# Kernel tuning notes

Hardware: AMD Instinct MI355X
Metric: run time of the kernel (lower is better)

The kernel has to match this reference:

```python
import jax, jax.numpy as jnp
import numpy as np

B, L, D, K = 32, 128, 400, 40
RTOL, ATOL = 1e-4, 1e-6


def setup_inputs() -> dict:
    key = jax.random.key(0)
    ks = jax.random.split(key, 9)
    s = 0.3                      # input scale keeps exp(energy) in fp32 range
    u = 1.0 / np.sqrt(D)         # param scale
    input_h = jax.random.normal(ks[0], (B, L, D), jnp.float32) * s
    input_c = jax.random.normal(ks[1], (B, L, D), jnp.float32) * s
    W_d = jax.random.normal(ks[2], (K, D), jnp.float32) * u
    W_e = jax.random.normal(ks[3], (K, D), jnp.float32) * u
    U = jax.random.normal(ks[4], (K, D, D), jnp.float32) * u
    b = jax.random.normal(ks[5], (K,), jnp.float32) * 0.1
    heads = jax.random.randint(ks[6], (B, L), 0, L)
    pos = jnp.arange(L)[None, :]
    heads = jnp.where(heads == pos, (heads + 1) % L, heads)  # no self-loops (diag is -inf)
    arc_tags = jax.random.randint(ks[7], (B, L), 0, K)
    lengths = jax.random.randint(ks[8], (B,), L // 2, L + 1)
    mask = (jnp.arange(L)[None, :] < lengths[:, None]).astype(jnp.float32)
    return {"input_h": input_h, "input_c": input_c, "W_d": W_d, "W_e": W_e,
            "U": U, "b": b, "mask": mask, "heads": heads,
            "arc_tags": arc_tags, "lengths": lengths}


def reference(input_h, input_c, W_d, W_e, U, b, mask, heads, arc_tags, lengths):
    Bsz, Ln, _ = input_h.shape
    # --- BiAAttention: energy[b,k,head,child] ---
    bil = jnp.einsum('bhd,kde,bce->bkhc', input_h, U, input_c)
    sd = jnp.einsum('kd,bhd->bkh', W_d, input_h)[:, :, :, None]   # head bias
    se = jnp.einsum('kd,bcd->bkc', W_e, input_c)[:, :, None, :]   # child bias
    energy = bil + sd + se + b[None, :, None, None]
    energy = energy * mask[:, None, :, None] * mask[:, None, None, :]
    eye = jnp.eye(Ln, dtype=energy.dtype)
    energy = energy + jnp.where(eye > 0, -jnp.inf, 0.0)           # no self-arcs
    # --- Matrix-Tree partition function ---
    A = jnp.exp(energy) * mask[:, None, :, None] * mask[:, None, None, :]
    A = A.sum(axis=1)                                             # [B,L,L] over labels
    Dg = A.sum(axis=1) * (1.0 + RTOL) + ATOL                      # column (in-degree) sums
    Lap = eye * Dg[:, None, :] - A                                # Laplacian
    Sub = Lap[:, 1:, 1:]                                          # drop root row/col
    valid = jnp.arange(Ln - 1)[None, :] < (lengths - 1)[:, None]
    vm = valid[:, :, None] & valid[:, None, :]
    Sub = jnp.where(vm, Sub, jnp.eye(Ln - 1, dtype=Sub.dtype))    # identity-pad = logdet of [1:len,1:len]
    z = jnp.linalg.slogdet(Sub)[1]                                # [B]
    # --- gold-tree energy ---
    bi = jnp.arange(Bsz)[:, None]
    pos = jnp.arange(Ln)[None, :]
    te = energy[bi, arc_tags, heads, pos]                         # [B,L]
    tgt = te[:, 1:].sum(axis=1)
    return z - tgt
```

## Files before the change

### kernel.cpp

```cpp
#include <hip/hip_runtime.h>
#include <hip/hip_bf16.h>

#define BB 32
#define LL 128
#define DD 400
#define KK 40
#define EE 416
#define SDN 50
#define SEN 52

typedef __attribute__((ext_vector_type(8)))  short  bfrag;
typedef __attribute__((ext_vector_type(16))) float  ffrag;

static __device__ __forceinline__ short f2bf(float f) {
    union { float f; unsigned u; } v; v.f = f;
    unsigned r = (v.u + 0x7FFF + ((v.u >> 16) & 1)) >> 16;
    return (short)r;
}

#define MFMA32(a, b, c) __builtin_amdgcn_mfma_f32_32x32x16_bf16((a), (b), (c), 0, 0, 0)

__global__ __launch_bounds__(256) void p_hc(
    const float* __restrict__ H, const float* __restrict__ C,
    short* __restrict__ Hs, short* __restrict__ Cs)
{
    int id = blockIdx.x * 256 + threadIdx.x;
    if (id < BB*SDN*LL) {
        int b = id / (SDN*LL); int r = id % (SDN*LL);
        int sd = r / LL; int h = r % LL;
        const float* src = H + ((size_t)(b*LL + h))*DD + sd*8;
        bfrag v;
#pragma unroll
        for (int j = 0; j < 8; ++j) v[j] = f2bf(src[j]);
        *(bfrag*)(Hs + (size_t)id*8) = v;
    } else {
        id -= BB*SDN*LL;
        int b = id / (SEN*LL); int r = id % (SEN*LL);
        int se = r / LL; int c = r % LL;
        bfrag v;
#pragma unroll
        for (int j = 0; j < 8; ++j) {
            int e = se*8 + j;
            v[j] = (e < DD) ? f2bf(C[((size_t)(b*LL + c))*DD + e]) : (short)0;
        }
        *(bfrag*)(Cs + (size_t)id*8) = v;
    }
}

__global__ __launch_bounds__(256) void p_u(
    const float* __restrict__ U, short* __restrict__ Us)
{
    int id = blockIdx.x * 256 + threadIdx.x;
    int k = id / (SDN*EE); int r = id % (SDN*EE);
    int sd = r / EE; int e = r % EE;
    bfrag v;
#pragma unroll
    for (int j = 0; j < 8; ++j)
        v[j] = (e < DD) ? f2bf(U[((size_t)k*DD + sd*8 + j)*DD + e]) : (short)0;
    *(bfrag*)(Us + (size_t)id*8) = v;
}

__global__ __launch_bounds__(256) void k_sdse(
    const float* __restrict__ H, const float* __restrict__ C,
    const float* __restrict__ Wd, const float* __restrict__ We,
    float* __restrict__ SD, float* __restrict__ SE)
{
    const int b   = blockIdx.x;
    const int rg  = blockIdx.y;
    const int srcC = blockIdx.z;
    const int t = threadIdx.x;

    __shared__ float Wl[KK*DD];
    {
        const float4* Wsrc = (const float4*)(srcC ? We : Wd);
        for (int i = t; i < KK*DD/4; i += 256) ((float4*)Wl)[i] = Wsrc[i];
    }
    __syncthreads();

    const int task = t >> 3;
    const int p    = t & 7;
    const int row  = rg*32 + task;
    const float* X = (srcC ? C : H) + ((size_t)(b*LL + row))*DD + p*50;

    float2 x[25];
#pragma unroll
    for (int i = 0; i < 25; ++i) x[i] = ((const float2*)X)[i];

    float* out = (srcC ? SE : SD) + (size_t)b*KK*LL + row;
    const float* Wb = Wl + p*50;

    for (int k = 0; k < KK; ++k) {
        const float2* wp = (const float2*)(Wb + k*DD);
        float s0 = 0.f, s1 = 0.f;
#pragma unroll
        for (int i = 0; i < 24; i += 2) {
            float2 w0 = wp[i], w1 = wp[i+1];
            s0 = fmaf(x[i].x,   w0.x, s0); s0 = fmaf(x[i].y,   w0.y, s0);
            s1 = fmaf(x[i+1].x, w1.x, s1); s1 = fmaf(x[i+1].y, w1.y, s1);
        }
        { float2 w0 = wp[24]; s0 = fmaf(x[24].x, w0.x, s0); s0 = fmaf(x[24].y, w0.y, s0); }
        float s = s0 + s1;
        s += __shfl_xor(s, 1); s += __shfl_xor(s, 2); s += __shfl_xor(s, 4);
        if (p == 0) out[k*LL] = s;
    }
}

__global__ __launch_bounds__(512, 4) void k_mfma(
    const short* __restrict__ Hs, const short* __restrict__ Cs,
    const short* __restrict__ Us,
    const float* __restrict__ SD, const float* __restrict__ SE,
    const float* __restrict__ bvec, const float* __restrict__ mask,
    const int* __restrict__ heads, const int* __restrict__ tags,
    float* __restrict__ A8, float* __restrict__ tgt)
{
    const int g  = blockIdx.x;
    const int b  = blockIdx.y;
    const int hh = blockIdx.z;
    const int t  = threadIdx.x;
    const int w  = t >> 6;
    const int l31 = t & 31;
    const int kh  = (t >> 5) & 1;

    __shared__ short Tbuf[52*64*8];

    const size_t hsB = (size_t)b * SDN * LL;
    const size_t csB = (size_t)b * SEN * LL;

    const int ht = w >> 2;
    const int ct = w & 3;
    const int hbase = 64*hh + 32*ht + 4*kh;
    const int c0 = 32*ct + l31;
    const float mc0 = mask[b*LL + c0];
    const int head0 = heads[b*LL + c0];
    const int tag0  = tags[b*LL + c0];
    unsigned vb = 0;
#pragma unroll
    for (int r = 0; r < 16; ++r) {
        const int hr = hbase + (r&3) + 8*(r>>2);
        if (mask[b*LL + hr] != 0.f && mc0 != 0.f && hr != c0) vb |= 1u << r;
    }

    ffrag E;
#pragma unroll
    for (int r = 0; r < 16; ++r) E[r] = 0.f;

    const int ntiles = (w < 2) ? 4 : 3;

    for (int kk = 0; kk < 5; ++kk) {
        const int k = g + 8*kk;
        const size_t usK = (size_t)k * SDN * EE;

        for (int ti = 0; ti < ntiles; ++ti) {
            const int tau = w + 8*ti;
            const int te = tau >> 1;
            const int th = tau & 1;
            const short* up = Us + (usK + (size_t)kh*EE + 32*te + l31)*8;
            const short* hp = Hs + (hsB + (size_t)kh*LL + 64*hh + 32*th + l31)*8;
#define UP(i) (*(const bfrag*)(up + (size_t)(i)*(2*EE*8)))
#define HP(i) (*(const bfrag*)(hp + (size_t)(i)*(2*LL*8)))
            ffrag T;
#pragma unroll
            for (int r = 0; r < 16; ++r) T[r] = 0.f;
            bfrag aA=UP(0), bA=HP(0), aB=UP(1), bB=HP(1);
            bfrag aL=UP(24), bL=HP(24);
#pragma unroll 1
            for (int j = 0; j < 11; ++j) {
                bfrag aC=UP(2*j+2), bC=HP(2*j+2);
                bfrag aD=UP(2*j+3), bD=HP(2*j+3);
                T = MFMA32(aA, bA, T);
                T = MFMA32(aB, bB, T);
                aA=aC; bA=bC; aB=aD; bB=bD;
            }
            T = MFMA32(aA, bA, T);
            T = MFMA32(aB, bB, T);
            T = MFMA32(aL, bL, T);
#undef UP
#undef HP
            const int hl = 32*th + l31;
#pragma unroll
            for (int r = 0; r < 16; r += 2) {
                const int e_loc = 32*te + (r&3) + 8*(r>>2) + 4*kh;
                const int s_e = e_loc >> 3, e7 = e_loc & 7;
                unsigned lo = (unsigned short)f2bf(T[r]);
                unsigned hi = (unsigned short)f2bf(T[r+1]);
                *(unsigned*)(&Tbuf[((size_t)s_e*64 + hl)*8 + e7]) = lo | (hi << 16);
            }
        }
        __syncthreads();

        ffrag S;
#pragma unroll
        for (int r = 0; r < 16; ++r) S[r] = 0.f;
        const short* tb = Tbuf + ((size_t)kh*64 + 32*ht + l31)*8;
        const short* cp = Cs + (csB + (size_t)kh*LL + c0)*8;
#define TB(es) (*(const bfrag*)(tb + (size_t)(es)*(2*64*8)))
#define CP(es) (*(const bfrag*)(cp + (size_t)(es)*(2*LL*8)))
        bfrag tA=TB(0), cA=CP(0), tB2=TB(1), cB=CP(1);
#pragma unroll 1
        for (int j = 0; j < 12; ++j) {
            bfrag tC=TB(2*j+2), cC=CP(2*j+2);
            bfrag tD=TB(2*j+3), cD=CP(2*j+3);
            S = MFMA32(tA,  cA, S);
            S = MFMA32(tB2, cB, S);
            tA=tC; cA=cC; tB2=tD; cB=cD;
        }
        S = MFMA32(tA,  cA, S);
        S = MFMA32(tB2, cB, S);
#undef TB
#undef CP

        const float bk = bvec[k];
        const float* SDb = SD + ((size_t)b*KK + k)*LL;
        const float sev = SE[((size_t)b*KK + k)*LL + c0];
#pragma unroll
        for (int r = 0; r < 16; ++r) {
            const int hr = hbase + (r&3) + 8*(r>>2);
            const float ev = S[r] + SDb[hr] + sev + bk;
            if ((vb >> r) & 1) {
                E[r] += __expf(ev);
                if (c0 >= 1 && tag0 == k && head0 == hr) atomicAdd(&tgt[b], ev);
            }
        }
        __syncthreads();
    }

    float* Ab = A8 + ((size_t)(g*BB + b))*LL*LL;
#pragma unroll
    for (int r = 0; r < 16; ++r) {
        const int hr = hbase + (r&3) + 8*(r>>2);
        Ab[hr*LL + c0] = E[r];
    }
}

__global__ __launch_bounds__(256) void k_logdet(
    const float* __restrict__ A8, const int* __restrict__ lengths,
    const float* __restrict__ tgt, float* __restrict__ out)
{
    const int b = blockIdx.x;
    const int t = threadIdx.x;
    const int rg = t >> 4;
    const int cg = t & 15;

    __shared__ float As[LL*LL];
    __shared__ float Dg[128];
    __shared__ float Lbuf[128];
    __shared__ float Ubuf[128];
    __shared__ float red[256];

    const float4* A4 = (const float4*)A8;
    for (int f4 = t; f4 < 4096; f4 += 256) {
        float4 s = make_float4(0.f, 0.f, 0.f, 0.f);
#pragma unroll
        for (int g = 0; g < 8; ++g) {
            float4 v = A4[((size_t)(g*BB + b))*4096 + f4];
            s.x += v.x; s.y += v.y; s.z += v.z; s.w += v.w;
        }
        ((float4*)As)[f4] = s;
    }
    __syncthreads();

    if (t < 128) {
        float s = 0.f;
        for (int hr = 0; hr < LL; ++hr) s += As[hr*LL + t];
        Dg[t] = s * (1.0f + 1e-4f) + 1e-6f;
    }
    __syncthreads();

    const int n1 = lengths[b] - 1;
    float m[8][8];
#pragma unroll
    for (int r = 0; r < 8; ++r) {
        const int i = 8*rg + r;
#pragma unroll
        for (int c = 0; c < 8; ++c) {
            const int j = 8*cg + c;
            float v;
            if (i < n1 && j < n1)
                v = ((i == j) ? Dg[i+1] : 0.f) - As[(i+1)*LL + (j+1)];
            else
                v = (i == j) ? 1.f : 0.f;
            m[r][c] = v;
        }
    }
    __syncthreads();

    for (int j = 0; j < 127; ++j) {
        const int jg = j >> 3, jl = j & 7;
        if (cg == jg) {
#pragma unroll
            for (int c = 0; c < 8; ++c) {
                if (c == jl) {
#pragma unroll
                    for (int r = 0; r < 8; ++r) Lbuf[8*rg + r] = m[r][c];
                }
            }
        }
        if (rg == jg) {
#pragma unroll
            for (int r = 0; r < 8; ++r) {
                if (r == jl) {
#pragma unroll
                    for (int c = 0; c < 8; ++c) Ubuf[8*cg + c] = m[r][c];
                }
            }
        }
        __syncthreads();

        const float piv = Lbuf[j];
        if (t == j) Dg[j] = piv;
        const float rp = 1.0f / piv;
        float lr[8], ur[8];
#pragma unroll
        for (int r = 0; r < 8; ++r) lr[r] = Lbuf[8*rg + r] * rp;
#pragma unroll
        for (int c = 0; c < 8; ++c) ur[c] = Ubuf[8*cg + c];
#pragma unroll
        for (int r = 0; r < 8; ++r)
#pragma unroll
            for (int c = 0; c < 8; ++c)
                m[r][c] = fmaf(-lr[r], ur[c], m[r][c]);
        __syncthreads();
    }

    float lsum = 0.f;
    if (t < 127) lsum = logf(Dg[t]);
    red[t] = lsum;
    __syncthreads();
    for (int off = 128; off >= 1; off >>= 1) {
        if (t < off) red[t] += red[t + off];
        __syncthreads();
    }
    if (t == 0) out[b] = red[0] - tgt[b];
}

extern "C" void kernel_launch(void* const* d_in, const int* in_sizes, int n_in,
                              void* d_out, int out_size, void* d_ws, size_t ws_size,
                              hipStream_t stream) {
    const float* H    = (const float*)d_in[0];
    const float* C    = (const float*)d_in[1];
    const float* Wd   = (const float*)d_in[2];
    const float* We   = (const float*)d_in[3];
    const float* U    = (const float*)d_in[4];
    const float* bv   = (const float*)d_in[5];
    const float* mask = (const float*)d_in[6];
    const int* heads  = (const int*)d_in[7];
    const int* tags   = (const int*)d_in[8];
    const int* lens   = (const int*)d_in[9];
    float* out = (float*)d_out;

    char* p = (char*)d_ws;
    float* A8  = (float*)p;                 p += (size_t)8*BB*LL*LL*4;
    float* tgt = (float*)p;                 p += 32*4;
    float* SDp = (float*)p;                 p += (size_t)BB*KK*LL*4;
    float* SEp = (float*)p;                 p += (size_t)BB*KK*LL*4;
    short* Hsp = (short*)p;                 p += (size_t)BB*SDN*LL*8*2;
    short* Csp = (short*)p;                 p += (size_t)BB*SEN*LL*8*2;
    short* Usp = (short*)p;                 p += (size_t)KK*SDN*EE*8*2;

    hipMemsetAsync(tgt, 0, 32*4, stream);

    p_hc  <<<dim3(1632), 256, 0, stream>>>(H, C, Hsp, Csp);
    p_u   <<<dim3(3250), 256, 0, stream>>>(U, Usp);
    k_sdse<<<dim3(BB, 4, 2), 256, 0, stream>>>(H, C, Wd, We, SDp, SEp);
    k_mfma<<<dim3(8, BB, 2), 512, 0, stream>>>(Hsp, Csp, Usp, SDp, SEp, bv, mask,
                                               heads, tags, A8, tgt);
    k_logdet<<<dim3(BB), 256, 0, stream>>>(A8, lens, tgt, out);
}
```

Before: 335.6 us.

## Merge head halves into 1024-thread blocks with LDS-staged H and 4-tile MFMA reuse

Fuses the two prep kernels into one launch. Restructures k_mfma so each block covers all 128 heads instead of splitting them across two blocks, so every U tile is read once per block instead of twice. H is staged into shared memory, and each wave computes four head tiles per U fragment. The intermediate T is written back into the same shared buffer for the second GEMM. The cost is half as many blocks (256 with 1024 threads), a larger 100KB LDS footprint, extra barriers, and only 13 of 16 waves doing the first GEMM.

```diff
diff --git a/kernel.cpp b/kernel.cpp
--- a/kernel.cpp
+++ b/kernel.cpp
@@ -20,9 +20,15 @@
 
 #define MFMA32(a, b, c) __builtin_amdgcn_mfma_f32_32x32x16_bf16((a), (b), (c), 0, 0, 0)
 
-__global__ __launch_bounds__(256) void p_hc(
+static __device__ __forceinline__ void fzero(ffrag& f) {
+#pragma unroll
+    for (int r = 0; r < 16; ++r) f[r] = 0.f;
+}
+
+__global__ __launch_bounds__(256) void p_prep(
     const float* __restrict__ H, const float* __restrict__ C,
-    short* __restrict__ Hs, short* __restrict__ Cs)
+    const float* __restrict__ U,
+    short* __restrict__ Hs, short* __restrict__ Cs, short* __restrict__ Us)
 {
     int id = blockIdx.x * 256 + threadIdx.x;
     if (id < BB*SDN*LL) {
@@ -33,7 +39,7 @@
 #pragma unroll
         for (int j = 0; j < 8; ++j) v[j] = f2bf(src[j]);
         *(bfrag*)(Hs + (size_t)id*8) = v;
-    } else {
+    } else if (id < BB*SDN*LL + BB*SEN*LL) {
         id -= BB*SDN*LL;
         int b = id / (SEN*LL); int r = id % (SEN*LL);
         int se = r / LL; int c = r % LL;
@@ -44,20 +50,16 @@
             v[j] = (e < DD) ? f2bf(C[((size_t)(b*LL + c))*DD + e]) : (short)0;
         }
         *(bfrag*)(Cs + (size_t)id*8) = v;
-    }
-}
-
-__global__ __launch_bounds__(256) void p_u(
-    const float* __restrict__ U, short* __restrict__ Us)
-{
-    int id = blockIdx.x * 256 + threadIdx.x;
-    int k = id / (SDN*EE); int r = id % (SDN*EE);
-    int sd = r / EE; int e = r % EE;
-    bfrag v;
-#pragma unroll
-    for (int j = 0; j < 8; ++j)
-        v[j] = (e < DD) ? f2bf(U[((size_t)k*DD + sd*8 + j)*DD + e]) : (short)0;
-    *(bfrag*)(Us + (size_t)id*8) = v;
+    } else {
+        id -= BB*SDN*LL + BB*SEN*LL;
+        int k = id / (SDN*EE); int r = id % (SDN*EE);
+        int sd = r / EE; int e = r % EE;
+        bfrag v;
+#pragma unroll
+        for (int j = 0; j < 8; ++j)
+            v[j] = (e < DD) ? f2bf(U[((size_t)k*DD + sd*8 + j)*DD + e]) : (short)0;
+        *(bfrag*)(Us + (size_t)id*8) = v;
+    }
 }
 
 __global__ __launch_bounds__(256) void k_sdse(
@@ -105,7 +107,22 @@
     }
 }
 
-__global__ __launch_bounds__(512, 4) void k_mfma(
+static __device__ __forceinline__ void t_write(
+    short* __restrict__ Ping, const ffrag& T, int et, int ht, int l31, int kh)
+{
+#pragma unroll
+    for (int r = 0; r < 16; r += 2) {
+        const int e_loc = 32*et + (r&3) + 8*(r>>2) + 4*kh;
+        if (e_loc < DD) {
+            unsigned lo = (unsigned short)f2bf(T[r]);
+            unsigned hi = (unsigned short)f2bf(T[r+1]);
+            *(unsigned*)(&Ping[((size_t)(e_loc>>3)*LL + 32*ht + l31)*8 + (e_loc&7)]) =
+                lo | (hi << 16);
+        }
+    }
+}
+
+__global__ __launch_bounds__(1024) void k_mfma(
     const short* __restrict__ Hs, const short* __restrict__ Cs,
     const short* __restrict__ Us,
     const float* __restrict__ SD, const float* __restrict__ SE,
@@ -115,20 +132,19 @@
 {
     const int g  = blockIdx.x;
     const int b  = blockIdx.y;
-    const int hh = blockIdx.z;
     const int t  = threadIdx.x;
     const int w  = t >> 6;
     const int l31 = t & 31;
     const int kh  = (t >> 5) & 1;
 
-    __shared__ short Tbuf[52*64*8];
+    __shared__ short Ping[SDN*LL*8];
 
     const size_t hsB = (size_t)b * SDN * LL;
     const size_t csB = (size_t)b * SEN * LL;
 
-    const int ht = w >> 2;
-    const int ct = w & 3;
-    const int hbase = 64*hh + 32*ht + 4*kh;
+    const int ht2 = w >> 2;
+    const int ct  = w & 3;
+    const int hbase = 32*ht2 + 4*kh;
     const int c0 = 32*ct + l31;
     const float mc0 = mask[b*LL + c0];
     const int head0 = heads[b*LL + c0];
@@ -140,74 +156,74 @@
         if (mask[b*LL + hr] != 0.f && mc0 != 0.f && hr != c0) vb |= 1u << r;
     }
 
-    ffrag E;
-#pragma unroll
-    for (int r = 0; r < 16; ++r) E[r] = 0.f;
-
-    const int ntiles = (w < 2) ? 4 : 3;
+    ffrag E; fzero(E);
 
     for (int kk = 0; kk < 5; ++kk) {
         const int k = g + 8*kk;
-        const size_t usK = (size_t)k * SDN * EE;
-
-        for (int ti = 0; ti < ntiles; ++ti) {
-            const int tau = w + 8*ti;
-            const int te = tau >> 1;
-            const int th = tau & 1;
-            const short* up = Us + (usK + (size_t)kh*EE + 32*te + l31)*8;
-            const short* hp = Hs + (hsB + (size_t)kh*LL + 64*hh + 32*th + l31)*8;
-#define UP(i) (*(const bfrag*)(up + (size_t)(i)*(2*EE*8)))
-#define HP(i) (*(const bfrag*)(hp + (size_t)(i)*(2*LL*8)))
-            ffrag T;
-#pragma unroll
-            for (int r = 0; r < 16; ++r) T[r] = 0.f;
-            bfrag aA=UP(0), bA=HP(0), aB=UP(1), bB=HP(1);
-            bfrag aL=UP(24), bL=HP(24);
+
+        __syncthreads();
+
+        {
+            const uint4* src = (const uint4*)(Hs + hsB*8);
+            uint4* dst = (uint4*)Ping;
+            for (int i = t; i < SDN*LL*8*2/16; i += 1024) dst[i] = src[i];
+        }
+        __syncthreads();
+
+        ffrag T0, T1, T2, T3;
+        if (w < 13) {
+            fzero(T0); fzero(T1); fzero(T2); fzero(T3);
+            const int et = w;
+            const short* up = Us + (((size_t)k*SDN + kh)*EE + 32*et + l31)*8;
+            const short* hb = Ping + ((size_t)kh*LL + l31)*8;
+#define UPF(j)    (*(const bfrag*)(up + (size_t)(j)*(2*EE*8)))
+#define HPF(j,ht) (*(const bfrag*)(hb + ((size_t)(2*(j))*LL + 32*(ht))*8))
+            bfrag a0 = UPF(0), a1 = UPF(1);
 #pragma unroll 1
-            for (int j = 0; j < 11; ++j) {
-                bfrag aC=UP(2*j+2), bC=HP(2*j+2);
-                bfrag aD=UP(2*j+3), bD=HP(2*j+3);
-                T = MFMA32(aA, bA, T);
-                T = MFMA32(aB, bB, T);
-                aA=aC; bA=bC; aB=aD; bB=bD;
-            }
-            T = MFMA32(aA, bA, T);
-            T = MFMA32(aB, bB, T);
-            T = MFMA32(aL, bL, T);
-#undef UP
-#undef HP
-            const int hl = 32*th + l31;
-#pragma unroll
-            for (int r = 0; r < 16; r += 2) {
-                const int e_loc = 32*te + (r&3) + 8*(r>>2) + 4*kh;
-                const int s_e = e_loc >> 3, e7 = e_loc & 7;
-                unsigned lo = (unsigned short)f2bf(T[r]);
-                unsigned hi = (unsigned short)f2bf(T[r+1]);
-                *(unsigned*)(&Tbuf[((size_t)s_e*64 + hl)*8 + e7]) = lo | (hi << 16);
-            }
-        }
-        __syncthreads();
-
-        ffrag S;
-#pragma unroll
-        for (int r = 0; r < 16; ++r) S[r] = 0.f;
-        const short* tb = Tbuf + ((size_t)kh*64 + 32*ht + l31)*8;
-        const short* cp = Cs + (csB + (size_t)kh*LL + c0)*8;
-#define TB(es) (*(const bfrag*)(tb + (size_t)(es)*(2*64*8)))
-#define CP(es) (*(const bfrag*)(cp + (size_t)(es)*(2*LL*8)))
-        bfrag tA=TB(0), cA=CP(0), tB2=TB(1), cB=CP(1);
+            for (int j = 0; j < 23; ++j) {
+                bfrag an = UPF(j+2);
+                bfrag b0 = HPF(j,0), b1 = HPF(j,1), b2 = HPF(j,2), b3 = HPF(j,3);
+                T0 = MFMA32(a0, b0, T0); T1 = MFMA32(a0, b1, T1);
+                T2 = MFMA32(a0, b2, T2); T3 = MFMA32(a0, b3, T3);
+                a0 = a1; a1 = an;
+            }
+            {
+                bfrag b0 = HPF(23,0), b1 = HPF(23,1), b2 = HPF(23,2), b3 = HPF(23,3);
+                T0 = MFMA32(a0, b0, T0); T1 = MFMA32(a0, b1, T1);
+                T2 = MFMA32(a0, b2, T2); T3 = MFMA32(a0, b3, T3);
+                b0 = HPF(24,0); b1 = HPF(24,1); b2 = HPF(24,2); b3 = HPF(24,3);
+                T0 = MFMA32(a1, b0, T0); T1 = MFMA32(a1, b1, T1);
+                T2 = MFMA32(a1, b2, T2); T3 = MFMA32(a1, b3, T3);
+            }
+#undef UPF
+#undef HPF
+        }
+        __syncthreads();
+
+        if (w < 13) {
+            t_write(Ping, T0, w, 0, l31, kh);
+            t_write(Ping, T1, w, 1, l31, kh);
+            t_write(Ping, T2, w, 2, l31, kh);
+            t_write(Ping, T3, w, 3, l31, kh);
+        }
+        __syncthreads();
+
+        ffrag S; fzero(S);
+        const short* ta = Ping + ((size_t)kh*LL + 32*ht2 + l31)*8;
+        const short* cp = Cs + (csB + (size_t)kh*LL + 32*ct + l31)*8;
+#define TAF(j) (*(const bfrag*)(ta + (size_t)(2*(j))*(LL*8)))
+#define CPF(j) (*(const bfrag*)(cp + (size_t)(2*(j))*(LL*8)))
+        bfrag c0f = CPF(0), c1f = CPF(1);
 #pragma unroll 1
-        for (int j = 0; j < 12; ++j) {
-            bfrag tC=TB(2*j+2), cC=CP(2*j+2);
-            bfrag tD=TB(2*j+3), cD=CP(2*j+3);
-            S = MFMA32(tA,  cA, S);
-            S = MFMA32(tB2, cB, S);
-            tA=tC; cA=cC; tB2=tD; cB=cD;
-        }
-        S = MFMA32(tA,  cA, S);
-        S = MFMA32(tB2, cB, S);
-#undef TB
-#undef CP
+        for (int j = 0; j < 23; ++j) {
+            bfrag cn = CPF(j+2);
+            S = MFMA32(TAF(j), c0f, S);
+            c0f = c1f; c1f = cn;
+        }
+        S = MFMA32(TAF(23), c0f, S);
+        S = MFMA32(TAF(24), c1f, S);
+#undef TAF
+#undef CPF
 
         const float bk = bvec[k];
         const float* SDb = SD + ((size_t)b*KK + k)*LL;
@@ -221,7 +237,6 @@
                 if (c0 >= 1 && tag0 == k && head0 == hr) atomicAdd(&tgt[b], ev);
             }
         }
-        __syncthreads();
     }
 
     float* Ab = A8 + ((size_t)(g*BB + b))*LL*LL;
@@ -359,10 +374,9 @@
 
     hipMemsetAsync(tgt, 0, 32*4, stream);
 
-    p_hc  <<<dim3(1632), 256, 0, stream>>>(H, C, Hsp, Csp);
-    p_u   <<<dim3(3250), 256, 0, stream>>>(U, Usp);
+    p_prep<<<dim3(4882), 256, 0, stream>>>(H, C, U, Hsp, Csp, Usp);
     k_sdse<<<dim3(BB, 4, 2), 256, 0, stream>>>(H, C, Wd, We, SDp, SEp);
-    k_mfma<<<dim3(8, BB, 2), 512, 0, stream>>>(Hsp, Csp, Usp, SDp, SEp, bv, mask,
-                                               heads, tags, A8, tgt);
+    k_mfma<<<dim3(8, BB), 1024, 0, stream>>>(Hsp, Csp, Usp, SDp, SEp, bv, mask,
+                                             heads, tags, A8, tgt);
     k_logdet<<<dim3(BB), 256, 0, stream>>>(A8, lens, tgt, out);
 }
```

Result: no change. 335.8 us (+0.0%).
